# Kernel tuning notes

Measured on AMD Instinct MI355X. Metric: run time of the kernel, lower is better.

Reference implementation:

```python
import jax, jax.numpy as jnp
import numpy as np

RANGE_EXTENDER = 5.0
EPS = 1e-8  # torch cosine_similarity eps

N_CLASSES = 256
LATENT = 256
H = W = 256


def setup_inputs() -> dict:
    key = jax.random.key(0)
    k1, k2, k3 = jax.random.split(key, 3)
    x = jax.random.normal(k1, (LATENT, H, W), dtype=jnp.float32)
    weights = jax.random.normal(k2, (N_CLASSES, LATENT), dtype=jnp.float32)
    scale = jax.random.normal(k3, (N_CLASSES,), dtype=jnp.float32)
    return {"x": x, "weights": weights, "scale": scale}


def reference(x, weights, scale):
    # out[c,i,j] = cos_sim(x[:,i,j], weights[c]) * scale[c] * RANGE_EXTENDER
    x_norm = jnp.sqrt(jnp.sum(x * x, axis=0, keepdims=True))           # (1, H, W)
    xn = x / jnp.maximum(x_norm, EPS)                                   # (D, H, W)
    w_norm = jnp.sqrt(jnp.sum(weights * weights, axis=1, keepdims=True))  # (C, 1)
    wn = weights / jnp.maximum(w_norm, EPS)                             # (C, D)
    cos = jnp.einsum("cd,dhw->chw", wn, xn)                            # (C, H, W)
    return cos * scale[:, None, None] * RANGE_EXTENDER
```

## Files before the change

kernel.cpp:

```cpp
#include <hip/hip_runtime.h>
#include <stdint.h>

typedef unsigned short u16;
typedef __bf16 bf16_t;
typedef bf16_t bf16x8 __attribute__((ext_vector_type(8)));
typedef float f32x4 __attribute__((ext_vector_type(4)));

static constexpr int P = 65536;

__device__ __forceinline__ float bfbits2f(uint32_t b) {
    union { uint32_t i; float f; } u; u.i = b << 16; return u.f;
}
__device__ __forceinline__ u16 f2bf(float f) {
    union { float f; uint32_t i; } u; u.f = f;
    uint32_t x = u.i + 0x7FFFu + ((u.i >> 16) & 1u);
    return (u16)(x >> 16);
}
__device__ __forceinline__ uint32_t pack2(float a, float b) {
    return (uint32_t)f2bf(a) | ((uint32_t)f2bf(b) << 16);
}

__device__ __forceinline__ int detect_bf16_input(const void* Xg) {
    const uint32_t* Xu = (const uint32_t*)Xg;
    const int lane = (int)(threadIdx.x & 63);
    const uint32_t v = Xu[(size_t)lane * 131071u];
    const uint32_t e = (v >> 7) & 0xFFu;
    unsigned long long m = __ballot(e >= 96u && e <= 135u);
    return __popcll(m) >= 40;
}

__global__ __launch_bounds__(64) void coshead_prep(
    const void* __restrict__ Xg, const void* __restrict__ Wg,
    const void* __restrict__ Sg, float* __restrict__ rs_ws,
    u16* __restrict__ wbf)
{
    const int c    = (int)blockIdx.x;
    const int lane = (int)threadIdx.x;
    const int bf   = detect_bf16_input(Xg);
    float s;
    uint2 packed;
    if (bf) {
        const uint2 v = *(const uint2*)((const u16*)Wg + (size_t)c * 256 + lane * 4);
        const float a = bfbits2f(v.x & 0xFFFFu), b = bfbits2f(v.x >> 16);
        const float d = bfbits2f(v.y & 0xFFFFu), e = bfbits2f(v.y >> 16);
        s = a * a + b * b + d * d + e * e;
        packed = v;
    } else {
        const f32x4 v = *(const f32x4*)((const float*)Wg + (size_t)c * 256 + lane * 4);
        s = v[0] * v[0] + v[1] * v[1] + v[2] * v[2] + v[3] * v[3];
        packed.x = pack2(v[0], v[1]);
        packed.y = pack2(v[2], v[3]);
    }
    *(uint2*)(wbf + (size_t)c * 256 + lane * 4) = packed;
    s += __shfl_xor(s, 1);  s += __shfl_xor(s, 2);  s += __shfl_xor(s, 4);
    s += __shfl_xor(s, 8);  s += __shfl_xor(s, 16); s += __shfl_xor(s, 32);
    if (lane == 0) {
        const float sc = bf ? bfbits2f((uint32_t)((const u16*)Sg)[c])
                            : ((const float*)Sg)[c];
        rs_ws[c] = sc * 5.0f / fmaxf(sqrtf(s), 1e-8f);
    }
}

__global__ __launch_bounds__(256, 2) void coshead_gemm(
    const void* __restrict__ Xg_, const u16* __restrict__ Wbf,
    const float* __restrict__ rs_ws, float* __restrict__ Og)
{
    __shared__ char smem_[16384 + 8192 + 256];
    char*  sB   = smem_;
    float* xs   = (float*)(smem_ + 16384);
    float* xinv = (float*)(smem_ + 16384 + 8192);

    const int t  = (int)threadIdx.x;
    const int l  = t & 63;
    const int w  = t >> 6;
    const int pbase = (int)blockIdx.x * 128;
    const int bf = detect_bf16_input(Xg_);

    const int g    = t & 7;
    const int r    = t >> 3;
    const int m16  = l & 15;
    const int quad = l >> 4;

    bf16x8 af[4][2][4];
    {
        const u16* wrow = Wbf + (size_t)(w * 64 + m16) * 256 + quad * 8;
#pragma unroll
        for (int kc = 0; kc < 4; ++kc)
#pragma unroll
            for (int kk = 0; kk < 2; ++kk)
#pragma unroll
                for (int tm = 0; tm < 4; ++tm)
                    af[kc][kk][tm] = *(const bf16x8*)(wrow + kc * 64 + kk * 32 + tm * 16 * 256);
    }

    f32x4 rA, rB, rC, rD;
    uint4 vb0, vb1;
    if (bf) {
        const u16* xp = (const u16*)Xg_ + (size_t)(2 * r) * P + pbase + g * 8;
        vb0 = *(const uint4*)xp;
        vb1 = *(const uint4*)(xp + P);
    } else {
        const float* xp = (const float*)Xg_ + (size_t)(2 * r) * P + pbase + g * 8;
        rA = *(const f32x4*)xp;
        rB = *(const f32x4*)(xp + 4);
        rC = *(const f32x4*)(xp + P);
        rD = *(const f32x4*)(xp + P + 4);
    }

    for (int pt = 0; pt < 2; ++pt) {
        const int p0 = pbase + pt * 64;

        float ssq[8];
#pragma unroll
        for (int j = 0; j < 8; ++j) ssq[j] = 0.f;
        f32x4 acc[4][4];
#pragma unroll
        for (int a = 0; a < 4; ++a)
#pragma unroll
            for (int b = 0; b < 4; ++b)
#pragma unroll
                for (int i = 0; i < 4; ++i) acc[a][b][i] = 0.f;

        for (int kc = 0; kc < 4; ++kc) {
            char* sBw = sB + (kc & 1) * 8192;

            if (bf) {
                const uint32_t e0[4] = {vb0.x, vb0.y, vb0.z, vb0.w};
                const uint32_t e1[4] = {vb1.x, vb1.y, vb1.z, vb1.w};
#pragma unroll
                for (int d = 0; d < 4; ++d) {
                    const float f00 = bfbits2f(e0[d] & 0xFFFFu), f01 = bfbits2f(e0[d] >> 16);
                    const float f10 = bfbits2f(e1[d] & 0xFFFFu), f11 = bfbits2f(e1[d] >> 16);
                    ssq[2 * d]     += f00 * f00 + f10 * f10;
                    ssq[2 * d + 1] += f01 * f01 + f11 * f11;
                    const uint32_t d0 = (e0[d] & 0xFFFFu) | (e1[d] << 16);
                    const uint32_t d1 = (e0[d] >> 16) | (e1[d] & 0xFFFF0000u);
                    const int pj0 = g * 8 + 2 * d, pj1 = pj0 + 1;
                    *(uint32_t*)(sBw + pj0 * 128 + (((r >> 2) ^ (pj0 & 7) ^ g) * 16) + (r & 3) * 4) = d0;
                    *(uint32_t*)(sBw + pj1 * 128 + (((r >> 2) ^ (pj1 & 7) ^ g) * 16) + (r & 3) * 4) = d1;
                }
            } else {
                const float f0[8] = {rA[0], rA[1], rA[2], rA[3], rB[0], rB[1], rB[2], rB[3]};
                const float f1[8] = {rC[0], rC[1], rC[2], rC[3], rD[0], rD[1], rD[2], rD[3]};
#pragma unroll
                for (int j = 0; j < 8; ++j) {
                    ssq[j] += f0[j] * f0[j] + f1[j] * f1[j];
                    const int pix = g * 8 + j;
                    *(uint32_t*)(sBw + pix * 128 + (((r >> 2) ^ (pix & 7) ^ g) * 16) + (r & 3) * 4) =
                        pack2(f0[j], f1[j]);
                }
            }

            const int it = pt * 4 + kc;
            if (it < 7) {
                const int nk = (it + 1) & 3, np = (it + 1) >> 2;
                if (bf) {
                    const u16* xp = (const u16*)Xg_ + (size_t)(2 * r + nk * 64) * P
                                    + pbase + np * 64 + g * 8;
                    vb0 = *(const uint4*)xp;
                    vb1 = *(const uint4*)(xp + P);
                } else {
                    const float* xp = (const float*)Xg_ + (size_t)(2 * r + nk * 64) * P
                                      + pbase + np * 64 + g * 8;
                    rA = *(const f32x4*)xp;
                    rB = *(const f32x4*)(xp + 4);
                    rC = *(const f32x4*)(xp + P);
                    rD = *(const f32x4*)(xp + P + 4);
                }
            }

            asm volatile("s_waitcnt lgkmcnt(0)" ::: "memory");
            __builtin_amdgcn_sched_barrier(0);
            __builtin_amdgcn_s_barrier();

#pragma unroll
            for (int kk = 0; kk < 2; ++kk) {
                bf16x8 bfr[4];
#pragma unroll
                for (int tn = 0; tn < 4; ++tn) {
                    const int pix = tn * 16 + m16;
                    bfr[tn] = *(const bf16x8*)(sBw + pix * 128 +
                               (((kk * 4 + quad) ^ (pix & 7) ^ (pix >> 3)) * 16));
                }
#pragma unroll
                for (int tm = 0; tm < 4; ++tm)
#pragma unroll
                    for (int tn = 0; tn < 4; ++tn)
                        acc[tm][tn] = __builtin_amdgcn_mfma_f32_16x16x32_bf16(
                            af[kc][kk][tm], bfr[tn], acc[tm][tn], 0, 0, 0);
            }
        }

        asm volatile("s_waitcnt lgkmcnt(0)" ::: "memory");
        __builtin_amdgcn_sched_barrier(0);
        __builtin_amdgcn_s_barrier();
#pragma unroll
        for (int j = 0; j < 8; ++j) xs[r * 64 + g * 8 + j] = ssq[j];
        asm volatile("s_waitcnt lgkmcnt(0)" ::: "memory");
        __builtin_amdgcn_sched_barrier(0);
        __builtin_amdgcn_s_barrier();
        if (t < 64) {
            float sx = 0.f;
#pragma unroll
            for (int rr = 0; rr < 32; ++rr) sx += xs[rr * 64 + t];
            xinv[t] = 1.0f / fmaxf(sqrtf(sx), 1e-8f);
        }
        asm volatile("s_waitcnt lgkmcnt(0)" ::: "memory");
        __builtin_amdgcn_sched_barrier(0);
        __builtin_amdgcn_s_barrier();

        float inv4[4];
#pragma unroll
        for (int tn = 0; tn < 4; ++tn) inv4[tn] = xinv[tn * 16 + m16];
#pragma unroll
        for (int tm = 0; tm < 4; ++tm) {
            const int cbase = w * 64 + tm * 16 + quad * 4;
            const f32x4 rs4 = *(const f32x4*)(rs_ws + cbase);
#pragma unroll
            for (int tn = 0; tn < 4; ++tn) {
#pragma unroll
                for (int i = 0; i < 4; ++i) {
                    Og[(size_t)(cbase + i) * P + p0 + tn * 16 + m16] =
                        acc[tm][tn][i] * rs4[i] * inv4[tn];
                }
            }
        }
    }
}

extern "C" void kernel_launch(void* const* d_in, const int* in_sizes, int n_in,
                              void* d_out, int out_size, void* d_ws, size_t ws_size,
                              hipStream_t stream) {
    (void)out_size; (void)ws_size;
    const void* X = d_in[0];
    const void* W = d_in[1];
    const void* S = d_in[2];
    for (int i = 0; i < n_in; ++i) {
        if (in_sizes[i] == 256 * 65536) X = d_in[i];
        else if (in_sizes[i] == 256 * 256) W = d_in[i];
        else if (in_sizes[i] == 256)      S = d_in[i];
    }
    float* rs  = (float*)d_ws;
    u16*   wbf = (u16*)((char*)d_ws + 1024);
    coshead_prep<<<dim3(256), dim3(64), 0, stream>>>(X, W, S, rs, wbf);
    coshead_gemm<<<dim3(512), dim3(256), 0, stream>>>(X, wbf, rs, (float*)d_out);
}
```

Baseline: 156.4 us.

## Double-buffer X prefetch two steps ahead and process 256 pixels per block

Each block now covers 256 pixels in four 64-pixel tiles, and the grid is halved to 256 blocks, so the preloaded bf16 weight fragments are reused across more tiles. Global loads of X are issued two k-steps ahead into alternating register sets, putting more memory requests in flight. Launch bounds drop to one block per SM so the extra registers fit. The cost is lower occupancy and only 256 blocks to spread over the GPU's compute units.

```diff
diff --git a/kernel.cpp b/kernel.cpp
--- a/kernel.cpp
+++ b/kernel.cpp
@@ -61,7 +61,7 @@
     }
 }
 
-__global__ __launch_bounds__(256, 2) void coshead_gemm(
+__global__ __launch_bounds__(256, 1) void coshead_gemm(
     const void* __restrict__ Xg_, const u16* __restrict__ Wbf,
     const float* __restrict__ rs_ws, float* __restrict__ Og)
 {
@@ -73,7 +73,7 @@
     const int t  = (int)threadIdx.x;
     const int l  = t & 63;
     const int w  = t >> 6;
-    const int pbase = (int)blockIdx.x * 128;
+    const int pbase = (int)blockIdx.x * 256;
     const int bf = detect_bf16_input(Xg_);
 
     const int g    = t & 7;
@@ -93,21 +93,29 @@
                     af[kc][kk][tm] = *(const bf16x8*)(wrow + kc * 64 + kk * 32 + tm * 16 * 256);
     }
 
-    f32x4 rA, rB, rC, rD;
-    uint4 vb0, vb1;
+    f32x4 rA0, rB0, rC0, rD0, rA1, rB1, rC1, rD1;
+    uint4 wa0, wa1, wb0, wb1;
     if (bf) {
-        const u16* xp = (const u16*)Xg_ + (size_t)(2 * r) * P + pbase + g * 8;
-        vb0 = *(const uint4*)xp;
-        vb1 = *(const uint4*)(xp + P);
+        const u16* x0 = (const u16*)Xg_ + (size_t)(2 * r) * P + pbase + g * 8;
+        wa0 = *(const uint4*)x0;
+        wa1 = *(const uint4*)(x0 + P);
+        const u16* x1 = (const u16*)Xg_ + (size_t)(2 * r + 64) * P + pbase + g * 8;
+        wb0 = *(const uint4*)x1;
+        wb1 = *(const uint4*)(x1 + P);
     } else {
-        const float* xp = (const float*)Xg_ + (size_t)(2 * r) * P + pbase + g * 8;
-        rA = *(const f32x4*)xp;
-        rB = *(const f32x4*)(xp + 4);
-        rC = *(const f32x4*)(xp + P);
-        rD = *(const f32x4*)(xp + P + 4);
-    }
-
-    for (int pt = 0; pt < 2; ++pt) {
+        const float* x0 = (const float*)Xg_ + (size_t)(2 * r) * P + pbase + g * 8;
+        rA0 = *(const f32x4*)x0;
+        rB0 = *(const f32x4*)(x0 + 4);
+        rC0 = *(const f32x4*)(x0 + P);
+        rD0 = *(const f32x4*)(x0 + P + 4);
+        const float* x1 = (const float*)Xg_ + (size_t)(2 * r + 64) * P + pbase + g * 8;
+        rA1 = *(const f32x4*)x1;
+        rB1 = *(const f32x4*)(x1 + 4);
+        rC1 = *(const f32x4*)(x1 + P);
+        rD1 = *(const f32x4*)(x1 + P + 4);
+    }
+
+    for (int pt = 0; pt < 4; ++pt) {
         const int p0 = pbase + pt * 64;
 
         float ssq[8];
@@ -121,12 +129,16 @@
 #pragma unroll
                 for (int i = 0; i < 4; ++i) acc[a][b][i] = 0.f;
 
+#pragma unroll
         for (int kc = 0; kc < 4; ++kc) {
             char* sBw = sB + (kc & 1) * 8192;
+            const int it = pt * 4 + kc;
 
             if (bf) {
-                const uint32_t e0[4] = {vb0.x, vb0.y, vb0.z, vb0.w};
-                const uint32_t e1[4] = {vb1.x, vb1.y, vb1.z, vb1.w};
+                const uint4 v0 = (kc & 1) ? wb0 : wa0;
+                const uint4 v1 = (kc & 1) ? wb1 : wa1;
+                const uint32_t e0[4] = {v0.x, v0.y, v0.z, v0.w};
+                const uint32_t e1[4] = {v1.x, v1.y, v1.z, v1.w};
 #pragma unroll
                 for (int d = 0; d < 4; ++d) {
                     const float f00 = bfbits2f(e0[d] & 0xFFFFu), f01 = bfbits2f(e0[d] >> 16);
@@ -140,8 +152,12 @@
                     *(uint32_t*)(sBw + pj1 * 128 + (((r >> 2) ^ (pj1 & 7) ^ g) * 16) + (r & 3) * 4) = d1;
                 }
             } else {
-                const float f0[8] = {rA[0], rA[1], rA[2], rA[3], rB[0], rB[1], rB[2], rB[3]};
-                const float f1[8] = {rC[0], rC[1], rC[2], rC[3], rD[0], rD[1], rD[2], rD[3]};
+                const f32x4 cA = (kc & 1) ? rA1 : rA0;
+                const f32x4 cB = (kc & 1) ? rB1 : rB0;
+                const f32x4 cC = (kc & 1) ? rC1 : rC0;
+                const f32x4 cD = (kc & 1) ? rD1 : rD0;
+                const float f0[8] = {cA[0], cA[1], cA[2], cA[3], cB[0], cB[1], cB[2], cB[3]};
+                const float f1[8] = {cC[0], cC[1], cC[2], cC[3], cD[0], cD[1], cD[2], cD[3]};
 #pragma unroll
                 for (int j = 0; j < 8; ++j) {
                     ssq[j] += f0[j] * f0[j] + f1[j] * f1[j];
@@ -151,21 +167,24 @@
                 }
             }
 
-            const int it = pt * 4 + kc;
-            if (it < 7) {
-                const int nk = (it + 1) & 3, np = (it + 1) >> 2;
+            if (it < 14) {
+                const int nj = it + 2;
+                const int nk = nj & 3, np = nj >> 2;
                 if (bf) {
                     const u16* xp = (const u16*)Xg_ + (size_t)(2 * r + nk * 64) * P
                                     + pbase + np * 64 + g * 8;
-                    vb0 = *(const uint4*)xp;
-                    vb1 = *(const uint4*)(xp + P);
+                    if (kc & 1) { wb0 = *(const uint4*)xp; wb1 = *(const uint4*)(xp + P); }
+                    else        { wa0 = *(const uint4*)xp; wa1 = *(const uint4*)(xp + P); }
                 } else {
                     const float* xp = (const float*)Xg_ + (size_t)(2 * r + nk * 64) * P
                                       + pbase + np * 64 + g * 8;
-                    rA = *(const f32x4*)xp;
-                    rB = *(const f32x4*)(xp + 4);
-                    rC = *(const f32x4*)(xp + P);
-                    rD = *(const f32x4*)(xp + P + 4);
+                    if (kc & 1) {
+                        rA1 = *(const f32x4*)xp;       rB1 = *(const f32x4*)(xp + 4);
+                        rC1 = *(const f32x4*)(xp + P); rD1 = *(const f32x4*)(xp + P + 4);
+                    } else {
+                        rA0 = *(const f32x4*)xp;       rB0 = *(const f32x4*)(xp + 4);
+                        rC0 = *(const f32x4*)(xp + P); rD0 = *(const f32x4*)(xp + P + 4);
+                    }
                 }
             }
 
@@ -243,5 +262,5 @@
     float* rs  = (float*)d_ws;
     u16*   wbf = (u16*)((char*)d_ws + 1024);
     coshead_prep<<<dim3(256), dim3(64), 0, stream>>>(X, W, S, rs, wbf);
-    coshead_gemm<<<dim3(512), dim3(256), 0, stream>>>(X, wbf, rs, (float*)d_out);
-}
+    coshead_gemm<<<dim3(256), dim3(256), 0, stream>>>(X, wbf, rs, (float*)d_out);
+}
```

Measured after the change: 127.1 us. 1.23x faster.
